# Performance work log

Hardware: AMD Instinct MI355X
Metric: run time of the kernel (lower is better)

## Reference

```python
import jax, jax.numpy as jnp
import numpy as np

E, FX, FE, H, OUT = 1_000_000, 32, 32, 64, 32
LN_EPS = 1e-5


def _ln(x, g, b):
    # LayerNorm over the channel (last) dim, elementwise_affine=True
    m = jnp.mean(x, axis=-1, keepdims=True)
    v = jnp.mean((x - m) ** 2, axis=-1, keepdims=True)
    return (x - m) * jax.lax.rsqrt(v + LN_EPS) * g + b


def setup_inputs() -> dict:
    key = jax.random.key(0)
    ks = jax.random.split(key, 6)
    d0 = 2 * FX + FE  # 96, the concat(src, dest, edge_attr) width
    src = jax.random.normal(ks[0], (E, FX), jnp.float32)
    dest = jax.random.normal(ks[1], (E, FX), jnp.float32)
    edge_attr = jax.random.normal(ks[2], (E, FE), jnp.float32)
    W1 = jax.random.normal(ks[3], (d0, H), jnp.float32) / np.float32(np.sqrt(d0))
    b1 = jnp.zeros((H,), jnp.float32)
    g1 = jnp.ones((H,), jnp.float32)
    be1 = jnp.zeros((H,), jnp.float32)
    W2 = jax.random.normal(ks[4], (H + d0, H), jnp.float32) / np.float32(np.sqrt(H + d0))
    b2 = jnp.zeros((H,), jnp.float32)
    g2 = jnp.ones((H,), jnp.float32)
    be2 = jnp.zeros((H,), jnp.float32)
    W3 = jax.random.normal(ks[5], (H, OUT), jnp.float32) / np.float32(np.sqrt(H))
    b3 = jnp.zeros((OUT,), jnp.float32)
    eb = jnp.zeros((E,), jnp.int32)  # edge-batch ids; unused (no GraphNorm in setup)
    return {"src": src, "dest": dest, "edge_attr": edge_attr,
            "W1": W1, "b1": b1, "g1": g1, "be1": be1,
            "W2": W2, "b2": b2, "g2": g2, "be2": be2,
            "W3": W3, "b3": b3, "eb": eb}


def reference(src, dest, edge_attr, W1, b1, g1, be1, W2, b2, g2, be2, W3, b3, eb):
    # out[0] = cat([src, dest, edge_attr], 1)
    x0 = jnp.concatenate([src, dest, edge_attr], axis=1)            # [E, 96]
    h = _ln(jax.nn.relu(x0 @ W1 + b1), g1, be1)                      # layers 0-2 -> [E, 64]
    # layer 3: shelf [3, 0] -> cat(out[3], out[0])
    h = _ln(jax.nn.relu(jnp.concatenate([h, x0], axis=1) @ W2 + b2), g2, be2)  # layers 3-5
    return h @ W3 + b3                                               # layer 6 -> [E, 32]
```

## Files before the change

### kernel.cpp

```cpp
#include <hip/hip_runtime.h>

typedef __bf16 bf16x8 __attribute__((ext_vector_type(8)));
typedef __bf16 bf16x4 __attribute__((ext_vector_type(4)));
typedef float  f32x4  __attribute__((ext_vector_type(4)));

#define HPAD 68
#define LDS_WAIT() asm volatile("s_waitcnt lgkmcnt(0)" ::: "memory")

static __device__ __forceinline__ bf16x8 ld_frag_lds(const __bf16* p) {
    bf16x4 lo = *(const bf16x4*)p;
    bf16x4 hi = *(const bf16x4*)(p + 4);
    bf16x8 r;
    r[0] = lo[0]; r[1] = lo[1]; r[2] = lo[2]; r[3] = lo[3];
    r[4] = hi[0]; r[5] = hi[1]; r[6] = hi[2]; r[7] = hi[3];
    return r;
}

static __device__ __forceinline__ bf16x8 ld_frag_g(const float* p) {
    float4 v0 = ((const float4*)p)[0];
    float4 v1 = ((const float4*)p)[1];
    bf16x8 r;
    r[0] = (__bf16)v0.x; r[1] = (__bf16)v0.y; r[2] = (__bf16)v0.z; r[3] = (__bf16)v0.w;
    r[4] = (__bf16)v1.x; r[5] = (__bf16)v1.y; r[6] = (__bf16)v1.z; r[7] = (__bf16)v1.w;
    return r;
}

static __device__ __forceinline__ void ln_epilogue(const f32x4* acc, const float* bv,
                                                   const float* gv, const float* ev,
                                                   __bf16* hp, int n16, int q) {
    float u[4][4];
    float sm[4] = {0.f, 0.f, 0.f, 0.f};
    float sq[4] = {0.f, 0.f, 0.f, 0.f};
#pragma unroll
    for (int t = 0; t < 4; ++t)
#pragma unroll
        for (int j = 0; j < 4; ++j) {
            float x = acc[t][j] + bv[t];
            x = fmaxf(x, 0.0f);
            u[t][j] = x;
            sm[j] += x;
            sq[j] += x * x;
        }
#pragma unroll
    for (int msk = 1; msk <= 8; msk <<= 1)
#pragma unroll
        for (int j = 0; j < 4; ++j) {
            sm[j] += __shfl_xor(sm[j], msk, 64);
            sq[j] += __shfl_xor(sq[j], msk, 64);
        }
    float mean[4], rstd[4];
#pragma unroll
    for (int j = 0; j < 4; ++j) {
        mean[j] = sm[j] * 0.015625f;
        float v = sq[j] * 0.015625f - mean[j] * mean[j];
        rstd[j] = rsqrtf(fmaxf(v, 0.0f) + 1e-5f);
    }
#pragma unroll
    for (int t = 0; t < 4; ++t)
#pragma unroll
        for (int j = 0; j < 4; ++j) {
            float y = (u[t][j] - mean[j]) * rstd[j] * gv[t] + ev[t];
            hp[(q * 4 + j) * HPAD + t * 16 + n16] = (__bf16)y;
        }
}

__global__ __launch_bounds__(256, 2)
void edge_model_kernel(const float* __restrict__ srcp,
                       const float* __restrict__ dstp,
                       const float* __restrict__ eap,
                       const float* __restrict__ W1, const float* __restrict__ b1,
                       const float* __restrict__ g1, const float* __restrict__ be1,
                       const float* __restrict__ W2, const float* __restrict__ b2,
                       const float* __restrict__ g2, const float* __restrict__ be2,
                       const float* __restrict__ W3, const float* __restrict__ b3,
                       float* __restrict__ out, int E) {
    __shared__ alignas(16) __bf16 hs[4][2][16 * HPAD];

    const int tid = threadIdx.x;
    const int w   = tid >> 6;
    const int l   = tid & 63;
    const int n16 = l & 15;
    const int q   = l >> 4;

    bf16x8 w1f[3][4];
    bf16x8 w2f[5][4];
    bf16x8 w3f[2][2];
#pragma unroll
    for (int s = 0; s < 3; ++s)
#pragma unroll
        for (int t = 0; t < 4; ++t) {
            bf16x8 f;
#pragma unroll
            for (int jj = 0; jj < 8; ++jj)
                f[jj] = (__bf16)W1[(s * 32 + q * 8 + jj) * 64 + t * 16 + n16];
            w1f[s][t] = f;
        }
#pragma unroll
    for (int s = 0; s < 5; ++s)
#pragma unroll
        for (int t = 0; t < 4; ++t) {
            bf16x8 f;
#pragma unroll
            for (int jj = 0; jj < 8; ++jj)
                f[jj] = (__bf16)W2[(s * 32 + q * 8 + jj) * 64 + t * 16 + n16];
            w2f[s][t] = f;
        }
#pragma unroll
    for (int s = 0; s < 2; ++s)
#pragma unroll
        for (int t = 0; t < 2; ++t) {
            bf16x8 f;
#pragma unroll
            for (int jj = 0; jj < 8; ++jj)
                f[jj] = (__bf16)W3[(s * 32 + q * 8 + jj) * 32 + t * 16 + n16];
            w3f[s][t] = f;
        }

    float b1v[4], g1v[4], e1v[4], b2v[4], g2v[4], e2v[4], b3v[2];
#pragma unroll
    for (int t = 0; t < 4; ++t) {
        int c = t * 16 + n16;
        b1v[t] = b1[c]; g1v[t] = g1[c]; e1v[t] = be1[c];
        b2v[t] = b2[c]; g2v[t] = g2[c]; e2v[t] = be2[c];
    }
    b3v[0] = b3[n16];
    b3v[1] = b3[16 + n16];

    const int nTiles = (E + 15) >> 4;
    const int stride = gridDim.x * 4;
    __bf16* h1p = &hs[w][0][0];
    __bf16* h2p = &hs[w][1][0];

    for (int tile = blockIdx.x * 4 + w; tile < nTiles; tile += stride) {
        const int e0 = tile << 4;
        const int rr = min(e0 + n16, E - 1);
        const size_t abase = (size_t)rr * 32 + q * 8;

        bf16x8 a0[3];
        a0[0] = ld_frag_g(srcp + abase);
        a0[1] = ld_frag_g(dstp + abase);
        a0[2] = ld_frag_g(eap + abase);

        f32x4 acc1[4] = {};
#pragma unroll
        for (int s = 0; s < 3; ++s)
#pragma unroll
            for (int t = 0; t < 4; ++t)
                acc1[t] = __builtin_amdgcn_mfma_f32_16x16x32_bf16(a0[s], w1f[s][t], acc1[t], 0, 0, 0);

        ln_epilogue(acc1, b1v, g1v, e1v, h1p, n16, q);
        LDS_WAIT();

        f32x4 acc2[4] = {};
        bf16x8 h1f0 = ld_frag_lds(h1p + n16 * HPAD + q * 8);
        bf16x8 h1f1 = ld_frag_lds(h1p + n16 * HPAD + 32 + q * 8);
#pragma unroll
        for (int t = 0; t < 4; ++t)
            acc2[t] = __builtin_amdgcn_mfma_f32_16x16x32_bf16(h1f0, w2f[0][t], acc2[t], 0, 0, 0);
#pragma unroll
        for (int t = 0; t < 4; ++t)
            acc2[t] = __builtin_amdgcn_mfma_f32_16x16x32_bf16(h1f1, w2f[1][t], acc2[t], 0, 0, 0);
#pragma unroll
        for (int s = 0; s < 3; ++s)
#pragma unroll
            for (int t = 0; t < 4; ++t)
                acc2[t] = __builtin_amdgcn_mfma_f32_16x16x32_bf16(a0[s], w2f[2 + s][t], acc2[t], 0, 0, 0);

        ln_epilogue(acc2, b2v, g2v, e2v, h2p, n16, q);
        LDS_WAIT();

        f32x4 acc3[2] = {};
#pragma unroll
        for (int s = 0; s < 2; ++s) {
            bf16x8 h2f = ld_frag_lds(h2p + n16 * HPAD + s * 32 + q * 8);
#pragma unroll
            for (int t = 0; t < 2; ++t)
                acc3[t] = __builtin_amdgcn_mfma_f32_16x16x32_bf16(h2f, w3f[s][t], acc3[t], 0, 0, 0);
        }

#pragma unroll
        for (int t = 0; t < 2; ++t)
#pragma unroll
            for (int j = 0; j < 4; ++j) {
                int r = e0 + q * 4 + j;
                if (r < E) out[(size_t)r * 32 + t * 16 + n16] = acc3[t][j] + b3v[t];
            }
    }
}

extern "C" void kernel_launch(void* const* d_in, const int* in_sizes, int n_in,
                              void* d_out, int out_size, void* d_ws, size_t ws_size,
                              hipStream_t stream) {
    (void)n_in; (void)out_size; (void)d_ws; (void)ws_size;
    const float* srcp = (const float*)d_in[0];
    const float* dstp = (const float*)d_in[1];
    const float* eap  = (const float*)d_in[2];
    const float* W1   = (const float*)d_in[3];
    const float* b1   = (const float*)d_in[4];
    const float* g1   = (const float*)d_in[5];
    const float* be1  = (const float*)d_in[6];
    const float* W2   = (const float*)d_in[7];
    const float* b2   = (const float*)d_in[8];
    const float* g2   = (const float*)d_in[9];
    const float* be2  = (const float*)d_in[10];
    const float* W3   = (const float*)d_in[11];
    const float* b3   = (const float*)d_in[12];
    float* out = (float*)d_out;

    const int E = in_sizes[0] / 32;
    const int nTiles = (E + 15) / 16;
    int blocks = (nTiles + 3) / 4;
    if (blocks > 512) blocks = 512;

    edge_model_kernel<<<blocks, 256, 0, stream>>>(srcp, dstp, eap, W1, b1, g1, be1,
                                                  W2, b2, g2, be2, W3, b3, out, E);
}
```

Measured before the change: 423.6 us.

## Stage weight fragments in LDS, prefetch next tile inputs, and widen blocks

Weight MFMA fragments move from per-thread registers into a shared LDS buffer that all waves of a block read, freeing many VGPRs so blocks can grow to 512 threads with higher occupancy bounds. The next tile's input rows are loaded into registers during the current tile's compute, a software prefetch meant to hide global memory latency. The cost is extra LDS reads for weights in every MFMA and one block-wide sync at startup.

```diff
diff --git a/kernel.cpp b/kernel.cpp
--- a/kernel.cpp
+++ b/kernel.cpp
@@ -4,10 +4,12 @@
 typedef __bf16 bf16x4 __attribute__((ext_vector_type(4)));
 typedef float  f32x4  __attribute__((ext_vector_type(4)));
 
+#define NW 8
 #define HPAD 68
+#define NFRAG 36
 #define LDS_WAIT() asm volatile("s_waitcnt lgkmcnt(0)" ::: "memory")
 
-static __device__ __forceinline__ bf16x8 ld_frag_lds(const __bf16* p) {
+static __device__ __forceinline__ bf16x8 ld_frag_lds8(const __bf16* p) {
     bf16x4 lo = *(const bf16x4*)p;
     bf16x4 hi = *(const bf16x4*)(p + 4);
     bf16x8 r;
@@ -16,9 +18,7 @@
     return r;
 }
 
-static __device__ __forceinline__ bf16x8 ld_frag_g(const float* p) {
-    float4 v0 = ((const float4*)p)[0];
-    float4 v1 = ((const float4*)p)[1];
+static __device__ __forceinline__ bf16x8 cvt_frag(float4 v0, float4 v1) {
     bf16x8 r;
     r[0] = (__bf16)v0.x; r[1] = (__bf16)v0.y; r[2] = (__bf16)v0.z; r[3] = (__bf16)v0.w;
     r[4] = (__bf16)v1.x; r[5] = (__bf16)v1.y; r[6] = (__bf16)v1.z; r[7] = (__bf16)v1.w;
@@ -64,7 +64,7 @@
         }
 }
 
-__global__ __launch_bounds__(256, 2)
+__global__ __launch_bounds__(512, 4)
 void edge_model_kernel(const float* __restrict__ srcp,
                        const float* __restrict__ dstp,
                        const float* __restrict__ eap,
@@ -74,7 +74,8 @@
                        const float* __restrict__ g2, const float* __restrict__ be2,
                        const float* __restrict__ W3, const float* __restrict__ b3,
                        float* __restrict__ out, int E) {
-    __shared__ alignas(16) __bf16 hs[4][2][16 * HPAD];
+    __shared__ alignas(16) __bf16 wlds[NFRAG * 64 * 8];
+    __shared__ alignas(16) __bf16 hs[NW][2][16 * HPAD];
 
     const int tid = threadIdx.x;
     const int w   = tid >> 6;
@@ -82,39 +83,18 @@
     const int n16 = l & 15;
     const int q   = l >> 4;
 
-    bf16x8 w1f[3][4];
-    bf16x8 w2f[5][4];
-    bf16x8 w3f[2][2];
-#pragma unroll
-    for (int s = 0; s < 3; ++s)
-#pragma unroll
-        for (int t = 0; t < 4; ++t) {
-            bf16x8 f;
-#pragma unroll
-            for (int jj = 0; jj < 8; ++jj)
-                f[jj] = (__bf16)W1[(s * 32 + q * 8 + jj) * 64 + t * 16 + n16];
-            w1f[s][t] = f;
-        }
-#pragma unroll
-    for (int s = 0; s < 5; ++s)
-#pragma unroll
-        for (int t = 0; t < 4; ++t) {
-            bf16x8 f;
-#pragma unroll
-            for (int jj = 0; jj < 8; ++jj)
-                f[jj] = (__bf16)W2[(s * 32 + q * 8 + jj) * 64 + t * 16 + n16];
-            w2f[s][t] = f;
-        }
-#pragma unroll
-    for (int s = 0; s < 2; ++s)
-#pragma unroll
-        for (int t = 0; t < 2; ++t) {
-            bf16x8 f;
-#pragma unroll
-            for (int jj = 0; jj < 8; ++jj)
-                f[jj] = (__bf16)W3[(s * 32 + q * 8 + jj) * 32 + t * 16 + n16];
-            w3f[s][t] = f;
-        }
+    for (int idx = tid; idx < NFRAG * 64; idx += blockDim.x) {
+        int fid = idx >> 6, fl = idx & 63;
+        int lq = fl >> 4, ln = fl & 15;
+        const float* Wsrc; int ldw, row0, col;
+        if (fid < 12)      { int s = fid >> 2,        t = fid & 3;        Wsrc = W1; ldw = 64; row0 = s * 32 + lq * 8; col = t * 16 + ln; }
+        else if (fid < 32) { int f = fid - 12, s = f >> 2, t = f & 3;     Wsrc = W2; ldw = 64; row0 = s * 32 + lq * 8; col = t * 16 + ln; }
+        else               { int f = fid - 32, s = f >> 1, t = f & 1;     Wsrc = W3; ldw = 32; row0 = s * 32 + lq * 8; col = t * 16 + ln; }
+        __bf16* dst = wlds + idx * 8;
+#pragma unroll
+        for (int jj = 0; jj < 8; ++jj)
+            dst[jj] = (__bf16)Wsrc[(row0 + jj) * ldw + col];
+    }
 
     float b1v[4], g1v[4], e1v[4], b2v[4], g2v[4], e2v[4], b3v[2];
 #pragma unroll
@@ -126,45 +106,70 @@
     b3v[0] = b3[n16];
     b3v[1] = b3[16 + n16];
 
+    __syncthreads();
+
     const int nTiles = (E + 15) >> 4;
-    const int stride = gridDim.x * 4;
+    const int stride = gridDim.x * NW;
     __bf16* h1p = &hs[w][0][0];
     __bf16* h2p = &hs[w][1][0];
-
-    for (int tile = blockIdx.x * 4 + w; tile < nTiles; tile += stride) {
+    const __bf16* wl = wlds + l * 8;
+
+    int tile = blockIdx.x * NW + w;
+    if (tile >= nTiles) return;
+
+    bf16x8 a0[3];
+    {
+        const size_t abase = (size_t)min((tile << 4) + n16, E - 1) * 32 + q * 8;
+        a0[0] = cvt_frag(((const float4*)(srcp + abase))[0], ((const float4*)(srcp + abase))[1]);
+        a0[1] = cvt_frag(((const float4*)(dstp + abase))[0], ((const float4*)(dstp + abase))[1]);
+        a0[2] = cvt_frag(((const float4*)(eap  + abase))[0], ((const float4*)(eap  + abase))[1]);
+    }
+
+    for (;;) {
         const int e0 = tile << 4;
-        const int rr = min(e0 + n16, E - 1);
-        const size_t abase = (size_t)rr * 32 + q * 8;
-
-        bf16x8 a0[3];
-        a0[0] = ld_frag_g(srcp + abase);
-        a0[1] = ld_frag_g(dstp + abase);
-        a0[2] = ld_frag_g(eap + abase);
+        const int nt = tile + stride;
+
+        const int pt = (nt < nTiles) ? nt : tile;
+        const size_t pbase = (size_t)min((pt << 4) + n16, E - 1) * 32 + q * 8;
+        float4 p0a = ((const float4*)(srcp + pbase))[0];
+        float4 p0b = ((const float4*)(srcp + pbase))[1];
+        float4 p1a = ((const float4*)(dstp + pbase))[0];
+        float4 p1b = ((const float4*)(dstp + pbase))[1];
+        float4 p2a = ((const float4*)(eap  + pbase))[0];
+        float4 p2b = ((const float4*)(eap  + pbase))[1];
 
         f32x4 acc1[4] = {};
 #pragma unroll
         for (int s = 0; s < 3; ++s)
 #pragma unroll
-            for (int t = 0; t < 4; ++t)
-                acc1[t] = __builtin_amdgcn_mfma_f32_16x16x32_bf16(a0[s], w1f[s][t], acc1[t], 0, 0, 0);
+            for (int t = 0; t < 4; ++t) {
+                bf16x8 wf = *(const bf16x8*)(wl + (s * 4 + t) * 512);
+                acc1[t] = __builtin_amdgcn_mfma_f32_16x16x32_bf16(a0[s], wf, acc1[t], 0, 0, 0);
+            }
 
         ln_epilogue(acc1, b1v, g1v, e1v, h1p, n16, q);
         LDS_WAIT();
 
         f32x4 acc2[4] = {};
-        bf16x8 h1f0 = ld_frag_lds(h1p + n16 * HPAD + q * 8);
-        bf16x8 h1f1 = ld_frag_lds(h1p + n16 * HPAD + 32 + q * 8);
-#pragma unroll
-        for (int t = 0; t < 4; ++t)
-            acc2[t] = __builtin_amdgcn_mfma_f32_16x16x32_bf16(h1f0, w2f[0][t], acc2[t], 0, 0, 0);
-#pragma unroll
-        for (int t = 0; t < 4; ++t)
-            acc2[t] = __builtin_amdgcn_mfma_f32_16x16x32_bf16(h1f1, w2f[1][t], acc2[t], 0, 0, 0);
+        bf16x8 h1f0 = ld_frag_lds8(h1p + n16 * HPAD + q * 8);
+        bf16x8 h1f1 = ld_frag_lds8(h1p + n16 * HPAD + 32 + q * 8);
+#pragma unroll
+        for (int t = 0; t < 4; ++t) {
+            bf16x8 wf = *(const bf16x8*)(wl + (12 + t) * 512);
+            acc2[t] = __builtin_amdgcn_mfma_f32_16x16x32_bf16(h1f0, wf, acc2[t], 0, 0, 0);
+        }
+#pragma unroll
+        for (int t = 0; t < 4; ++t) {
+            bf16x8 wf = *(const bf16x8*)(wl + (16 + t) * 512);
+            acc2[t] = __builtin_amdgcn_mfma_f32_16x16x32_bf16(h1f1, wf, acc2[t], 0, 0, 0);
+        }
 #pragma unroll
         for (int s = 0; s < 3; ++s)
 #pragma unroll
-            for (int t = 0; t < 4; ++t)
-                acc2[t] = __builtin_amdgcn_mfma_f32_16x16x32_bf16(a0[s], w2f[2 + s][t], acc2[t], 0, 0, 0);
+            for (int t = 0; t < 4; ++t) {
+                bf16x8 wf = *(const bf16x8*)(wl + (20 + s * 4 + t) * 512);
+                acc2[t] = __builtin_amdgcn_mfma_f32_16x16x32_bf16(a0[s], wf, acc2[t], 0, 0, 0);
+            }
 
         ln_epilogue(acc2, b2v, g2v, e2v, h2p, n16, q);
         LDS_WAIT();
@@ -172,10 +177,12 @@
         f32x4 acc3[2] = {};
 #pragma unroll
         for (int s = 0; s < 2; ++s) {
-            bf16x8 h2f = ld_frag_lds(h2p + n16 * HPAD + s * 32 + q * 8);
-#pragma unroll
-            for (int t = 0; t < 2; ++t)
-                acc3[t] = __builtin_amdgcn_mfma_f32_16x16x32_bf16(h2f, w3f[s][t], acc3[t], 0, 0, 0);
+            bf16x8 h2f = ld_frag_lds8(h2p + n16 * HPAD + s * 32 + q * 8);
+#pragma unroll
+            for (int t = 0; t < 2; ++t) {
+                bf16x8 wf = *(const bf16x8*)(wl + (32 + s * 2 + t) * 512);
+                acc3[t] = __builtin_amdgcn_mfma_f32_16x16x32_bf16(h2f, wf, acc3[t], 0, 0, 0);
+            }
         }
 
 #pragma unroll
@@ -185,6 +192,12 @@
                 int r = e0 + q * 4 + j;
                 if (r < E) out[(size_t)r * 32 + t * 16 + n16] = acc3[t][j] + b3v[t];
             }
+
+        if (nt >= nTiles) break;
+        tile = nt;
+        a0[0] = cvt_frag(p0a, p0b);
+        a0[1] = cvt_frag(p1a, p1b);
+        a0[2] = cvt_frag(p2a, p2b);
     }
 }
 
@@ -209,9 +222,9 @@
 
     const int E = in_sizes[0] / 32;
     const int nTiles = (E + 15) / 16;
-    int blocks = (nTiles + 3) / 4;
+    int blocks = (nTiles + NW - 1) / NW;
     if (blocks > 512) blocks = 512;
 
-    edge_model_kernel<<<blocks, 256, 0, stream>>>(srcp, dstp, eap, W1, b1, g1, be1,
+    edge_model_kernel<<<blocks, 512, 0, stream>>>(srcp, dstp, eap, W1, b1, g1, be1,
                                                   W2, b2, g2, be2, W3, b3, out, E);
 }
```

Measured after the change: 409.0 us. 3.4% less time.
